# Kernel tuning notes

Hardware: AMD Instinct MI355X
Metric: run time of the kernel (lower is better)

## Reference

```python
import jax, jax.numpy as jnp
import numpy as np
from jax import lax


def _maxpool(x, kh, kw):
    # max_pool2d with stride 1 and 'same' padding (kh//2, kw//2)
    return lax.reduce_window(
        x, -jnp.inf, lax.max,
        window_dimensions=(1, 1, kh, kw),
        window_strides=(1, 1, 1, 1),
        padding=[(0, 0), (0, 0), (kh // 2, kh // 2), (kw // 2, kw // 2)])


def _minpool(x, kh, kw):
    # -max_pool2d(-x) == min pooling
    return lax.reduce_window(
        x, jnp.inf, lax.min,
        window_dimensions=(1, 1, kh, kw),
        window_strides=(1, 1, 1, 1),
        padding=[(0, 0), (0, 0), (kh // 2, kh // 2), (kw // 2, kw // 2)])


def soft_erode(img):
    p1 = _minpool(img, 3, 1)
    p2 = _minpool(img, 1, 3)
    return jnp.minimum(p1, p2)


def soft_dilate(img):
    return _maxpool(img, 3, 3)


def soft_open(img):
    return soft_dilate(soft_erode(img))


def setup_inputs() -> dict:
    key = jax.random.key(0)
    img = jax.random.uniform(key, (16, 1, 1024, 1024), dtype=jnp.float32)
    return {"img": img, "num_iter": 10}


def reference(img, num_iter):
    # soft skeleton via iterative thinning
    skel = jax.nn.relu(img - soft_open(img))
    img_eroded = img
    for _ in range(num_iter):  # fixed small trip count (static)
        img_eroded = soft_erode(img_eroded)
        delta = jax.nn.relu(img_eroded - soft_open(img_eroded))
        skel = skel + jax.nn.relu(delta - skel * delta)
    return skel
```

## Files before the change

kernel.cpp:

```cpp
#include <hip/hip_runtime.h>
#include <hip/hip_fp16.h>


#define W 1024
#define H 1024
#define NBATCH 16
#define RV 8

__device__ __forceinline__ uint32_t HMIN2(uint32_t a, uint32_t b) {
  uint32_t d;
  asm("v_pk_min_f16 %0, %1, %2" : "=v"(d) : "v"(a), "v"(b));
  return d;
}
__device__ __forceinline__ uint32_t HMAX2(uint32_t a, uint32_t b) {
  uint32_t d;
  asm("v_pk_max_f16 %0, %1, %2" : "=v"(d) : "v"(a), "v"(b));
  return d;
}
__device__ __forceinline__ uint32_t PKSUB(uint32_t a, uint32_t b) {
  uint32_t d;
  asm("v_pk_add_f16 %0, %1, %2 neg_lo:[0,1] neg_hi:[0,1]"
      : "=v"(d) : "v"(a), "v"(b));
  return d;
}
__device__ __forceinline__ uint32_t PKMUL(uint32_t a, uint32_t b) {
  uint32_t d;
  asm("v_pk_mul_f16 %0, %1, %2" : "=v"(d) : "v"(a), "v"(b));
  return d;
}
__device__ __forceinline__ uint32_t PKRELU(uint32_t a) {
  uint32_t d;
  asm("v_pk_max_f16 %0, %1, 0" : "=v"(d) : "v"(a));
  return d;
}
__device__ __forceinline__ uint32_t PK(float x, float y) {
  __half2 h = __floats2half2_rn(x, y);
  return *(uint32_t*)&h;
}
__device__ __forceinline__ float CVTLO(uint32_t u) {
  uint16_t t = (uint16_t)(u & 0xffffu);
  __half h = *(__half*)&t;
  return __half2float(h);
}
__device__ __forceinline__ float CVTHI(uint32_t u) {
  uint16_t t = (uint16_t)(u >> 16);
  __half h = *(__half*)&t;
  return __half2float(h);
}
__device__ __forceinline__ uint32_t SHUP(uint32_t x) {
  return (uint32_t)__builtin_amdgcn_update_dpp(0, (int)x, 0x138, 0xf, 0xf,
                                               true);
}
__device__ __forceinline__ uint32_t SHDN(uint32_t x) {
  return (uint32_t)__builtin_amdgcn_update_dpp(0, (int)x, 0x130, 0xf, 0xf,
                                               true);
}

#define STEP(P, C, N, DOH, DOU, K, INIT) {                                  \
  const uint32_t ca = F##C##a, cb = F##C##b;                                \
  const uint32_t na = F##N##a, nb = F##N##b;                                \
  const uint32_t vma = HMIN2(HMIN2(PMa, ca), na);                           \
  const uint32_t vmb = HMIN2(HMIN2(PMb, cb), nb);                           \
  const uint32_t t = SHUP(cb);                                              \
  const uint32_t r = SHDN(ca);                                              \
  const uint32_t m1 = mL ? (ca & 0xffffu) : (t >> 16);                      \
  const uint32_t r4 = mR ? (cb >> 16) : (r & 0xffffu);                      \
  const uint32_t sla = (ca >> 16) | (cb << 16);                             \
  const uint32_t slb = (cb >> 16) | (r4 << 16);                             \
  const uint32_t sra = m1 | (ca << 16);                                     \
  const uint32_t ea = HMIN2(vma, HMIN2(sra, sla));                          \
  const uint32_t eb = HMIN2(vmb, HMIN2(sla, slb));                          \
  if (DOH) {                                                                \
    const uint32_t te = SHUP(eb);                                           \
    const uint32_t re = SHDN(ea);                                           \
    const uint32_t em1 = mL ? (ea & 0xffffu) : (te >> 16);                  \
    const uint32_t er4 = mR ? (eb >> 16) : (re & 0xffffu);                  \
    const uint32_t esla = (ea >> 16) | (eb << 16);                          \
    const uint32_t eslb = (eb >> 16) | (er4 << 16);                         \
    const uint32_t esra = em1 | (ea << 16);                                 \
    const uint32_t hca = HMAX2(ea, HMAX2(esra, esla));                      \
    const uint32_t hcb = HMAX2(eb, HMAX2(esla, eslb));                      \
    if (DOU) {                                                              \
      uint32_t haa = h2a, hab = h2b, hba = hca, hbb = hcb;                  \
      if (K == 0 && top) { haa = h1a; hab = h1b; }                          \
      if (K == RV - 1 && bot) { hba = h1a; hbb = h1b; }                     \
      const uint32_t dda = HMAX2(HMAX2(haa, h1a), hba);                     \
      const uint32_t ddb = HMAX2(HMAX2(hab, h1b), hbb);                     \
      const uint32_t fa = PKSUB(ONE2, PKRELU(PKSUB(PMa, dda)));             \
      const uint32_t fb = PKSUB(ONE2, PKRELU(PKSUB(PMb, ddb)));             \
      if (INIT) { Q##K##a = fa; Q##K##b = fb; }                             \
      else { Q##K##a = PKMUL(Q##K##a, fa); Q##K##b = PKMUL(Q##K##b, fb); }  \
    }                                                                       \
    h2a = h1a; h2b = h1b; h1a = hca; h1b = hcb;                             \
  }                                                                         \
  F##P##a = ea; F##P##b = eb;                                               \
  PMa = ca; PMb = cb;                                                       \
}

#define STAGE_BEGIN uint32_t PMa = F0a, PMb = F0b,                          \
    h1a = 0, h1b = 0, h2a = 0, h2b = 0;

#define S_V22(INIT) { STAGE_BEGIN                                           \
  STEP(0,1,2,0,0,0,INIT)  STEP(1,2,3,0,0,0,INIT)  STEP(2,3,4,0,0,0,INIT)    \
  STEP(3,4,5,0,0,0,INIT)  STEP(4,5,6,0,0,0,INIT)                            \
  STEP(5,6,7,1,0,0,INIT)  STEP(6,7,8,1,0,0,INIT)                            \
  STEP(7,8,9,1,1,0,INIT)  STEP(8,9,10,1,1,1,INIT) STEP(9,10,11,1,1,2,INIT)  \
  STEP(10,11,12,1,1,3,INIT) STEP(11,12,13,1,1,4,INIT)                       \
  STEP(12,13,14,1,1,5,INIT) STEP(13,14,15,1,1,6,INIT)                       \
  STEP(14,15,16,1,1,7,INIT)                                                 \
  STEP(15,16,17,0,0,0,INIT) STEP(16,17,18,0,0,0,INIT)                       \
  STEP(17,18,19,0,0,0,INIT) STEP(18,19,20,0,0,0,INIT)                       \
  STEP(19,20,21,0,0,0,INIT) }

#define S_V20 { STAGE_BEGIN                                                 \
  STEP(0,1,2,0,0,0,0)   STEP(1,2,3,0,0,0,0)   STEP(2,3,4,0,0,0,0)           \
  STEP(3,4,5,0,0,0,0)                                                       \
  STEP(4,5,6,1,0,0,0)   STEP(5,6,7,1,0,0,0)                                 \
  STEP(6,7,8,1,1,0,0)   STEP(7,8,9,1,1,1,0)   STEP(8,9,10,1,1,2,0)          \
  STEP(9,10,11,1,1,3,0) STEP(10,11,12,1,1,4,0) STEP(11,12,13,1,1,5,0)       \
  STEP(12,13,14,1,1,6,0) STEP(13,14,15,1,1,7,0)                             \
  STEP(14,15,16,0,0,0,0) STEP(15,16,17,0,0,0,0) STEP(16,17,18,0,0,0,0)      \
  STEP(17,18,19,0,0,0,0) }

#define S_V18 { STAGE_BEGIN                                                 \
  STEP(0,1,2,0,0,0,0)   STEP(1,2,3,0,0,0,0)   STEP(2,3,4,0,0,0,0)           \
  STEP(3,4,5,1,0,0,0)   STEP(4,5,6,1,0,0,0)                                 \
  STEP(5,6,7,1,1,0,0)   STEP(6,7,8,1,1,1,0)   STEP(7,8,9,1,1,2,0)           \
  STEP(8,9,10,1,1,3,0)  STEP(9,10,11,1,1,4,0) STEP(10,11,12,1,1,5,0)        \
  STEP(11,12,13,1,1,6,0) STEP(12,13,14,1,1,7,0)                             \
  STEP(13,14,15,0,0,0,0) STEP(14,15,16,0,0,0,0) STEP(15,16,17,0,0,0,0) }

#define S_V16 { STAGE_BEGIN                                                 \
  STEP(0,1,2,0,0,0,0)   STEP(1,2,3,0,0,0,0)                                 \
  STEP(2,3,4,1,0,0,0)   STEP(3,4,5,1,0,0,0)                                 \
  STEP(4,5,6,1,1,0,0)   STEP(5,6,7,1,1,1,0)   STEP(6,7,8,1,1,2,0)           \
  STEP(7,8,9,1,1,3,0)   STEP(8,9,10,1,1,4,0)  STEP(9,10,11,1,1,5,0)         \
  STEP(10,11,12,1,1,6,0) STEP(11,12,13,1,1,7,0)                             \
  STEP(12,13,14,0,0,0,0) STEP(13,14,15,0,0,0,0) }

#define S_V14 { STAGE_BEGIN                                                 \
  STEP(0,1,2,0,0,0,0)                                                       \
  STEP(1,2,3,1,0,0,0)   STEP(2,3,4,1,0,0,0)                                 \
  STEP(3,4,5,1,1,0,0)   STEP(4,5,6,1,1,1,0)   STEP(5,6,7,1,1,2,0)           \
  STEP(6,7,8,1,1,3,0)   STEP(7,8,9,1,1,4,0)   STEP(8,9,10,1,1,5,0)          \
  STEP(9,10,11,1,1,6,0) STEP(10,11,12,1,1,7,0)                              \
  STEP(11,12,13,0,0,0,0) }

#define S_V12 { STAGE_BEGIN                                                 \
  STEP(0,1,2,1,0,0,0)   STEP(1,2,3,1,0,0,0)                                 \
  STEP(2,3,4,1,1,0,0)   STEP(3,4,5,1,1,1,0)   STEP(4,5,6,1,1,2,0)           \
  STEP(5,6,7,1,1,3,0)   STEP(6,7,8,1,1,4,0)   STEP(7,8,9,1,1,5,0)           \
  STEP(8,9,10,1,1,6,0)  STEP(9,10,11,1,1,7,0) }

#define DECLF(i) uint32_t F##i##a, F##i##b;

#define COMMON_SETUP                                                        \
  const int l = threadIdx.x & 63;                                           \
  const int wid = threadIdx.x >> 6;                                         \
  const int w = blockIdx.x;                                                 \
  const int y0 = (blockIdx.y * 4 + wid) * RV;                               \
  const size_t base = (size_t)blockIdx.z * (size_t)(W * H);                 \
  const int rx = 208 * w - 8 + 4 * l;                                       \
  const int cq = min(max(rx, 0), W - 4);                                    \
  const bool mL = (rx == 0);                                                \
  const bool mR = (rx == W - 4);                                            \
  const bool top = (y0 == 0);                                               \
  const bool bot = (y0 + RV == H);                                          \
  const int wend = min(208 * (w + 1), W);                                   \
  const bool wr = (rx >= 208 * w) && (rx < wend);                           \
  const uint32_t ONE2 = 0x3C003C00u;

__global__ __launch_bounds__(256) void skel6(const float* __restrict__ in,
                                             uint16_t* __restrict__ e16,
                                             uint16_t* __restrict__ q16) {
  COMMON_SETUP
  DECLF(0) DECLF(1) DECLF(2) DECLF(3) DECLF(4) DECLF(5) DECLF(6) DECLF(7)
  DECLF(8) DECLF(9) DECLF(10) DECLF(11) DECLF(12) DECLF(13) DECLF(14)
  DECLF(15) DECLF(16) DECLF(17) DECLF(18) DECLF(19) DECLF(20) DECLF(21)
  uint32_t Q0a, Q0b, Q1a, Q1b, Q2a, Q2b, Q3a, Q3b;
  uint32_t Q4a, Q4b, Q5a, Q5b, Q6a, Q6b, Q7a, Q7b;

#define LOADROW1(i) {                                                       \
    const int gy = min(max(y0 - 7 + i, 0), H - 1);                          \
    const float4 v = *(const float4*)(in + base + (size_t)gy * W + cq);     \
    F##i##a = PK(v.x, v.y); F##i##b = PK(v.z, v.w); }
  LOADROW1(0) LOADROW1(1) LOADROW1(2) LOADROW1(3) LOADROW1(4) LOADROW1(5)
  LOADROW1(6) LOADROW1(7) LOADROW1(8) LOADROW1(9) LOADROW1(10) LOADROW1(11)
  LOADROW1(12) LOADROW1(13) LOADROW1(14) LOADROW1(15) LOADROW1(16)
  LOADROW1(17) LOADROW1(18) LOADROW1(19) LOADROW1(20) LOADROW1(21)
#undef LOADROW1

  S_V22(1) S_V20 S_V18 S_V16 S_V14 S_V12

  if (wr) {
#define STOREQ(k) {                                                         \
      *(uint2*)(q16 + base + (size_t)(y0 + k) * W + rx) =                   \
          make_uint2(Q##k##a, Q##k##b); }
    STOREQ(0) STOREQ(1) STOREQ(2) STOREQ(3)
    STOREQ(4) STOREQ(5) STOREQ(6) STOREQ(7)
#undef STOREQ
#define STOREE(k, j) {                                                      \
      *(uint2*)(e16 + base + (size_t)(y0 + k) * W + rx) =                   \
          make_uint2(F##j##a, F##j##b); }
    STOREE(0, 1) STOREE(1, 2) STOREE(2, 3) STOREE(3, 4)
    STOREE(4, 5) STOREE(5, 6) STOREE(6, 7) STOREE(7, 8)
#undef STOREE
  }
}

__global__ __launch_bounds__(256) void skel5(const uint16_t* __restrict__ e16,
                                             const uint16_t* __restrict__ q16,
                                             float* __restrict__ skel) {
  COMMON_SETUP
  DECLF(0) DECLF(1) DECLF(2) DECLF(3) DECLF(4) DECLF(5) DECLF(6) DECLF(7)
  DECLF(8) DECLF(9) DECLF(10) DECLF(11) DECLF(12) DECLF(13) DECLF(14)
  DECLF(15) DECLF(16) DECLF(17) DECLF(18) DECLF(19)
  uint32_t Q0a, Q0b, Q1a, Q1b, Q2a, Q2b, Q3a, Q3b;
  uint32_t Q4a, Q4b, Q5a, Q5b, Q6a, Q6b, Q7a, Q7b;

#define LOADROW2(i) {                                                       \
    const int gy = min(max(y0 - 6 + i, 0), H - 1);                          \
    const uint2 v = *(const uint2*)(e16 + base + (size_t)gy * W + cq);      \
    F##i##a = v.x; F##i##b = v.y; }
  LOADROW2(0) LOADROW2(1) LOADROW2(2) LOADROW2(3) LOADROW2(4) LOADROW2(5)
  LOADROW2(6) LOADROW2(7) LOADROW2(8) LOADROW2(9) LOADROW2(10) LOADROW2(11)
  LOADROW2(12) LOADROW2(13) LOADROW2(14) LOADROW2(15) LOADROW2(16)
  LOADROW2(17) LOADROW2(18) LOADROW2(19)
#undef LOADROW2

#define LOADQ(k) {                                                          \
    const uint2 v = *(const uint2*)(q16 + base + (size_t)(y0 + k) * W + cq); \
    Q##k##a = v.x; Q##k##b = v.y; }
  LOADQ(0) LOADQ(1) LOADQ(2) LOADQ(3) LOADQ(4) LOADQ(5) LOADQ(6) LOADQ(7)
#undef LOADQ

  S_V20 S_V18 S_V16 S_V14 S_V12

  if (wr) {
#define STOREQ(k) {                                                         \
      float4 s;                                                             \
      s.x = 1.0f - CVTLO(Q##k##a); s.y = 1.0f - CVTHI(Q##k##a);             \
      s.z = 1.0f - CVTLO(Q##k##b); s.w = 1.0f - CVTHI(Q##k##b);             \
      *(float4*)(skel + base + (size_t)(y0 + k) * W + rx) = s; }
    STOREQ(0) STOREQ(1) STOREQ(2) STOREQ(3)
    STOREQ(4) STOREQ(5) STOREQ(6) STOREQ(7)
#undef STOREQ
  }
}

extern "C" void kernel_launch(void* const* d_in, const int* in_sizes, int n_in,
                              void* d_out, int out_size, void* d_ws,
                              size_t ws_size, hipStream_t stream) {
  const float* img = (const float*)d_in[0];
  float* skel = (float*)d_out;
  const size_t NPIX = (size_t)NBATCH * W * H;
  uint16_t* E = (uint16_t*)d_ws;
  uint16_t* Q = E + NPIX;

  dim3 grid(5, H / (4 * RV), NBATCH);
  skel6<<<grid, 256, 0, stream>>>(img, E, Q);
  skel5<<<grid, 256, 0, stream>>>(E, Q, skel);
}
```

Before: 102.5 us.

## Split fused skeleton pipeline into three kernels with shallower row halos

The 11-stage erosion/open chain moves from two kernels (6+5 stages) to three (4+4+3 stages), with erosion and Q state passed through workspace in fp16. Each kernel now loads fewer halo rows (18/18/16 instead of 22/20), which cuts redundant recomputation, register pressure and halo loads. The cost is an extra kernel launch and an extra global round trip for the intermediate E and Q buffers, plus a larger workspace.

```diff
diff --git a/kernel.cpp b/kernel.cpp
--- a/kernel.cpp
+++ b/kernel.cpp
@@ -100,35 +100,15 @@
 #define STAGE_BEGIN uint32_t PMa = F0a, PMb = F0b,                          \
     h1a = 0, h1b = 0, h2a = 0, h2b = 0;
 
-#define S_V22(INIT) { STAGE_BEGIN                                           \
-  STEP(0,1,2,0,0,0,INIT)  STEP(1,2,3,0,0,0,INIT)  STEP(2,3,4,0,0,0,INIT)    \
-  STEP(3,4,5,0,0,0,INIT)  STEP(4,5,6,0,0,0,INIT)                            \
-  STEP(5,6,7,1,0,0,INIT)  STEP(6,7,8,1,0,0,INIT)                            \
-  STEP(7,8,9,1,1,0,INIT)  STEP(8,9,10,1,1,1,INIT) STEP(9,10,11,1,1,2,INIT)  \
-  STEP(10,11,12,1,1,3,INIT) STEP(11,12,13,1,1,4,INIT)                       \
-  STEP(12,13,14,1,1,5,INIT) STEP(13,14,15,1,1,6,INIT)                       \
-  STEP(14,15,16,1,1,7,INIT)                                                 \
-  STEP(15,16,17,0,0,0,INIT) STEP(16,17,18,0,0,0,INIT)                       \
-  STEP(17,18,19,0,0,0,INIT) STEP(18,19,20,0,0,0,INIT)                       \
-  STEP(19,20,21,0,0,0,INIT) }
-
-#define S_V20 { STAGE_BEGIN                                                 \
-  STEP(0,1,2,0,0,0,0)   STEP(1,2,3,0,0,0,0)   STEP(2,3,4,0,0,0,0)           \
-  STEP(3,4,5,0,0,0,0)                                                       \
-  STEP(4,5,6,1,0,0,0)   STEP(5,6,7,1,0,0,0)                                 \
-  STEP(6,7,8,1,1,0,0)   STEP(7,8,9,1,1,1,0)   STEP(8,9,10,1,1,2,0)          \
-  STEP(9,10,11,1,1,3,0) STEP(10,11,12,1,1,4,0) STEP(11,12,13,1,1,5,0)       \
-  STEP(12,13,14,1,1,6,0) STEP(13,14,15,1,1,7,0)                             \
-  STEP(14,15,16,0,0,0,0) STEP(15,16,17,0,0,0,0) STEP(16,17,18,0,0,0,0)      \
-  STEP(17,18,19,0,0,0,0) }
-
-#define S_V18 { STAGE_BEGIN                                                 \
-  STEP(0,1,2,0,0,0,0)   STEP(1,2,3,0,0,0,0)   STEP(2,3,4,0,0,0,0)           \
-  STEP(3,4,5,1,0,0,0)   STEP(4,5,6,1,0,0,0)                                 \
-  STEP(5,6,7,1,1,0,0)   STEP(6,7,8,1,1,1,0)   STEP(7,8,9,1,1,2,0)           \
-  STEP(8,9,10,1,1,3,0)  STEP(9,10,11,1,1,4,0) STEP(10,11,12,1,1,5,0)        \
-  STEP(11,12,13,1,1,6,0) STEP(12,13,14,1,1,7,0)                             \
-  STEP(13,14,15,0,0,0,0) STEP(14,15,16,0,0,0,0) STEP(15,16,17,0,0,0,0) }
+#define S_V18(INIT) { STAGE_BEGIN                                           \
+  STEP(0,1,2,0,0,0,INIT)   STEP(1,2,3,0,0,0,INIT)   STEP(2,3,4,0,0,0,INIT)  \
+  STEP(3,4,5,1,0,0,INIT)   STEP(4,5,6,1,0,0,INIT)                           \
+  STEP(5,6,7,1,1,0,INIT)   STEP(6,7,8,1,1,1,INIT)   STEP(7,8,9,1,1,2,INIT)  \
+  STEP(8,9,10,1,1,3,INIT)  STEP(9,10,11,1,1,4,INIT)                         \
+  STEP(10,11,12,1,1,5,INIT) STEP(11,12,13,1,1,6,INIT)                       \
+  STEP(12,13,14,1,1,7,INIT)                                                 \
+  STEP(13,14,15,0,0,0,INIT) STEP(14,15,16,0,0,0,INIT)                       \
+  STEP(15,16,17,0,0,0,INIT) }
 
 #define S_V16 { STAGE_BEGIN                                                 \
   STEP(0,1,2,0,0,0,0)   STEP(1,2,3,0,0,0,0)                                 \
@@ -170,72 +150,113 @@
   const bool wr = (rx >= 208 * w) && (rx < wend);                           \
   const uint32_t ONE2 = 0x3C003C00u;
 
-__global__ __launch_bounds__(256) void skel6(const float* __restrict__ in,
-                                             uint16_t* __restrict__ e16,
+#define DECL_ALL_F18                                                        \
+  DECLF(0) DECLF(1) DECLF(2) DECLF(3) DECLF(4) DECLF(5) DECLF(6) DECLF(7)   \
+  DECLF(8) DECLF(9) DECLF(10) DECLF(11) DECLF(12) DECLF(13) DECLF(14)       \
+  DECLF(15) DECLF(16) DECLF(17)
+#define DECL_ALL_Q                                                          \
+  uint32_t Q0a, Q0b, Q1a, Q1b, Q2a, Q2b, Q3a, Q3b;                          \
+  uint32_t Q4a, Q4b, Q5a, Q5b, Q6a, Q6b, Q7a, Q7b;
+
+#define LOADQ_ALL(qp)                                                       \
+  { const uint2 v = *(const uint2*)(qp + base + (size_t)(y0 + 0) * W + cq); \
+    Q0a = v.x; Q0b = v.y; }                                                 \
+  { const uint2 v = *(const uint2*)(qp + base + (size_t)(y0 + 1) * W + cq); \
+    Q1a = v.x; Q1b = v.y; }                                                 \
+  { const uint2 v = *(const uint2*)(qp + base + (size_t)(y0 + 2) * W + cq); \
+    Q2a = v.x; Q2b = v.y; }                                                 \
+  { const uint2 v = *(const uint2*)(qp + base + (size_t)(y0 + 3) * W + cq); \
+    Q3a = v.x; Q3b = v.y; }                                                 \
+  { const uint2 v = *(const uint2*)(qp + base + (size_t)(y0 + 4) * W + cq); \
+    Q4a = v.x; Q4b = v.y; }                                                 \
+  { const uint2 v = *(const uint2*)(qp + base + (size_t)(y0 + 5) * W + cq); \
+    Q5a = v.x; Q5b = v.y; }                                                 \
+  { const uint2 v = *(const uint2*)(qp + base + (size_t)(y0 + 6) * W + cq); \
+    Q6a = v.x; Q6b = v.y; }                                                 \
+  { const uint2 v = *(const uint2*)(qp + base + (size_t)(y0 + 7) * W + cq); \
+    Q7a = v.x; Q7b = v.y; }
+
+#define STOREQ16_ALL(qp)                                                    \
+  *(uint2*)(qp + base + (size_t)(y0 + 0) * W + rx) = make_uint2(Q0a, Q0b);  \
+  *(uint2*)(qp + base + (size_t)(y0 + 1) * W + rx) = make_uint2(Q1a, Q1b);  \
+  *(uint2*)(qp + base + (size_t)(y0 + 2) * W + rx) = make_uint2(Q2a, Q2b);  \
+  *(uint2*)(qp + base + (size_t)(y0 + 3) * W + rx) = make_uint2(Q3a, Q3b);  \
+  *(uint2*)(qp + base + (size_t)(y0 + 4) * W + rx) = make_uint2(Q4a, Q4b);  \
+  *(uint2*)(qp + base + (size_t)(y0 + 5) * W + rx) = make_uint2(Q5a, Q5b);  \
+  *(uint2*)(qp + base + (size_t)(y0 + 6) * W + rx) = make_uint2(Q6a, Q6b);  \
+  *(uint2*)(qp + base + (size_t)(y0 + 7) * W + rx) = make_uint2(Q7a, Q7b);
+
+#define STOREE_ALL(ep)                                                      \
+  *(uint2*)(ep + base + (size_t)(y0 + 0) * W + rx) = make_uint2(F1a, F1b);  \
+  *(uint2*)(ep + base + (size_t)(y0 + 1) * W + rx) = make_uint2(F2a, F2b);  \
+  *(uint2*)(ep + base + (size_t)(y0 + 2) * W + rx) = make_uint2(F3a, F3b);  \
+  *(uint2*)(ep + base + (size_t)(y0 + 3) * W + rx) = make_uint2(F4a, F4b);  \
+  *(uint2*)(ep + base + (size_t)(y0 + 4) * W + rx) = make_uint2(F5a, F5b);  \
+  *(uint2*)(ep + base + (size_t)(y0 + 5) * W + rx) = make_uint2(F6a, F6b);  \
+  *(uint2*)(ep + base + (size_t)(y0 + 6) * W + rx) = make_uint2(F7a, F7b);  \
+  *(uint2*)(ep + base + (size_t)(y0 + 7) * W + rx) = make_uint2(F8a, F8b);
+
+__global__ __launch_bounds__(256) void skelA(const float* __restrict__ in,
+                                             uint16_t* __restrict__ e4,
                                              uint16_t* __restrict__ q16) {
   COMMON_SETUP
-  DECLF(0) DECLF(1) DECLF(2) DECLF(3) DECLF(4) DECLF(5) DECLF(6) DECLF(7)
-  DECLF(8) DECLF(9) DECLF(10) DECLF(11) DECLF(12) DECLF(13) DECLF(14)
-  DECLF(15) DECLF(16) DECLF(17) DECLF(18) DECLF(19) DECLF(20) DECLF(21)
-  uint32_t Q0a, Q0b, Q1a, Q1b, Q2a, Q2b, Q3a, Q3b;
-  uint32_t Q4a, Q4b, Q5a, Q5b, Q6a, Q6b, Q7a, Q7b;
-
-#define LOADROW1(i) {                                                       \
-    const int gy = min(max(y0 - 7 + i, 0), H - 1);                          \
+  DECL_ALL_F18
+  DECL_ALL_Q
+#define LOADROW(i) {                                                        \
+    const int gy = min(max(y0 - 5 + i, 0), H - 1);                          \
     const float4 v = *(const float4*)(in + base + (size_t)gy * W + cq);     \
     F##i##a = PK(v.x, v.y); F##i##b = PK(v.z, v.w); }
-  LOADROW1(0) LOADROW1(1) LOADROW1(2) LOADROW1(3) LOADROW1(4) LOADROW1(5)
-  LOADROW1(6) LOADROW1(7) LOADROW1(8) LOADROW1(9) LOADROW1(10) LOADROW1(11)
-  LOADROW1(12) LOADROW1(13) LOADROW1(14) LOADROW1(15) LOADROW1(16)
-  LOADROW1(17) LOADROW1(18) LOADROW1(19) LOADROW1(20) LOADROW1(21)
-#undef LOADROW1
-
-  S_V22(1) S_V20 S_V18 S_V16 S_V14 S_V12
-
+  LOADROW(0) LOADROW(1) LOADROW(2) LOADROW(3) LOADROW(4) LOADROW(5)
+  LOADROW(6) LOADROW(7) LOADROW(8) LOADROW(9) LOADROW(10) LOADROW(11)
+  LOADROW(12) LOADROW(13) LOADROW(14) LOADROW(15) LOADROW(16) LOADROW(17)
+#undef LOADROW
+  S_V18(1) S_V16 S_V14 S_V12
   if (wr) {
-#define STOREQ(k) {                                                         \
-      *(uint2*)(q16 + base + (size_t)(y0 + k) * W + rx) =                   \
-          make_uint2(Q##k##a, Q##k##b); }
-    STOREQ(0) STOREQ(1) STOREQ(2) STOREQ(3)
-    STOREQ(4) STOREQ(5) STOREQ(6) STOREQ(7)
-#undef STOREQ
-#define STOREE(k, j) {                                                      \
-      *(uint2*)(e16 + base + (size_t)(y0 + k) * W + rx) =                   \
-          make_uint2(F##j##a, F##j##b); }
-    STOREE(0, 1) STOREE(1, 2) STOREE(2, 3) STOREE(3, 4)
-    STOREE(4, 5) STOREE(5, 6) STOREE(6, 7) STOREE(7, 8)
-#undef STOREE
+    STOREQ16_ALL(q16)
+    STOREE_ALL(e4)
   }
 }
 
-__global__ __launch_bounds__(256) void skel5(const uint16_t* __restrict__ e16,
+__global__ __launch_bounds__(256) void skelB(const uint16_t* __restrict__ e4,
+                                             uint16_t* __restrict__ e8,
+                                             uint16_t* __restrict__ q16) {
+  COMMON_SETUP
+  DECL_ALL_F18
+  DECL_ALL_Q
+#define LOADROW(i) {                                                        \
+    const int gy = min(max(y0 - 5 + i, 0), H - 1);                          \
+    const uint2 v = *(const uint2*)(e4 + base + (size_t)gy * W + cq);       \
+    F##i##a = v.x; F##i##b = v.y; }
+  LOADROW(0) LOADROW(1) LOADROW(2) LOADROW(3) LOADROW(4) LOADROW(5)
+  LOADROW(6) LOADROW(7) LOADROW(8) LOADROW(9) LOADROW(10) LOADROW(11)
+  LOADROW(12) LOADROW(13) LOADROW(14) LOADROW(15) LOADROW(16) LOADROW(17)
+#undef LOADROW
+  LOADQ_ALL(q16)
+  S_V18(0) S_V16 S_V14 S_V12
+  if (wr) {
+    STOREQ16_ALL(q16)
+    STOREE_ALL(e8)
+  }
+}
+
+__global__ __launch_bounds__(256) void skelC(const uint16_t* __restrict__ e8,
                                              const uint16_t* __restrict__ q16,
                                              float* __restrict__ skel) {
   COMMON_SETUP
   DECLF(0) DECLF(1) DECLF(2) DECLF(3) DECLF(4) DECLF(5) DECLF(6) DECLF(7)
   DECLF(8) DECLF(9) DECLF(10) DECLF(11) DECLF(12) DECLF(13) DECLF(14)
-  DECLF(15) DECLF(16) DECLF(17) DECLF(18) DECLF(19)
-  uint32_t Q0a, Q0b, Q1a, Q1b, Q2a, Q2b, Q3a, Q3b;
-  uint32_t Q4a, Q4b, Q5a, Q5b, Q6a, Q6b, Q7a, Q7b;
-
-#define LOADROW2(i) {                                                       \
-    const int gy = min(max(y0 - 6 + i, 0), H - 1);                          \
-    const uint2 v = *(const uint2*)(e16 + base + (size_t)gy * W + cq);      \
+  DECLF(15)
+  DECL_ALL_Q
+#define LOADROW(i) {                                                        \
+    const int gy = min(max(y0 - 4 + i, 0), H - 1);                          \
+    const uint2 v = *(const uint2*)(e8 + base + (size_t)gy * W + cq);       \
     F##i##a = v.x; F##i##b = v.y; }
-  LOADROW2(0) LOADROW2(1) LOADROW2(2) LOADROW2(3) LOADROW2(4) LOADROW2(5)
-  LOADROW2(6) LOADROW2(7) LOADROW2(8) LOADROW2(9) LOADROW2(10) LOADROW2(11)
-  LOADROW2(12) LOADROW2(13) LOADROW2(14) LOADROW2(15) LOADROW2(16)
-  LOADROW2(17) LOADROW2(18) LOADROW2(19)
-#undef LOADROW2
-
-#define LOADQ(k) {                                                          \
-    const uint2 v = *(const uint2*)(q16 + base + (size_t)(y0 + k) * W + cq); \
-    Q##k##a = v.x; Q##k##b = v.y; }
-  LOADQ(0) LOADQ(1) LOADQ(2) LOADQ(3) LOADQ(4) LOADQ(5) LOADQ(6) LOADQ(7)
-#undef LOADQ
-
-  S_V20 S_V18 S_V16 S_V14 S_V12
-
+  LOADROW(0) LOADROW(1) LOADROW(2) LOADROW(3) LOADROW(4) LOADROW(5)
+  LOADROW(6) LOADROW(7) LOADROW(8) LOADROW(9) LOADROW(10) LOADROW(11)
+  LOADROW(12) LOADROW(13) LOADROW(14) LOADROW(15)
+#undef LOADROW
+  LOADQ_ALL(q16)
+  S_V16 S_V14 S_V12
   if (wr) {
 #define STOREQ(k) {                                                         \
       float4 s;                                                             \
@@ -254,10 +275,12 @@
   const float* img = (const float*)d_in[0];
   float* skel = (float*)d_out;
   const size_t NPIX = (size_t)NBATCH * W * H;
-  uint16_t* E = (uint16_t*)d_ws;
-  uint16_t* Q = E + NPIX;
+  uint16_t* E4 = (uint16_t*)d_ws;
+  uint16_t* E8 = E4 + NPIX;
+  uint16_t* Q = E8 + NPIX;
 
   dim3 grid(5, H / (4 * RV), NBATCH);
-  skel6<<<grid, 256, 0, stream>>>(img, E, Q);
-  skel5<<<grid, 256, 0, stream>>>(E, Q, skel);
-}
+  skelA<<<grid, 256, 0, stream>>>(img, E4, Q);
+  skelB<<<grid, 256, 0, stream>>>(E4, E8, Q);
+  skelC<<<grid, 256, 0, stream>>>(E8, Q, skel);
+}
```

New measurement: 113.0 us. +10.2%, slower.
